# Kernel tuning notes

Hardware: AMD Instinct MI355X
Metric: run time of the kernel (lower is better)

The kernel has to match this reference:

```python
import jax, jax.numpy as jnp
from jax import lax
import numpy as np

MAX_K = 9  # alpha<1 -> kernel_size = 2*floor(floor(8*alpha)/2)+1 <= 9
SIGMA2 = 256.0  # sigma=16


def conv3x3(x, w, b):
    # reflection pad 1 + VALID 3x3 conv (torch cross-correlation == lax default)
    xp = jnp.pad(x, ((0, 0), (0, 0), (1, 1), (1, 1)), mode='reflect')
    y = lax.conv_general_dilated(xp, w, (1, 1), 'VALID')
    return y + b[None, :, None, None]


def up2(x):
    return jnp.repeat(jnp.repeat(x, 2, axis=2), 2, axis=3)


def get_hh(x):
    # x - nearest_upsample(avg_pool2(x)); H,W even
    B, C, H, W = x.shape
    p = x.reshape(B, C, H // 2, 2, W // 2, 2).mean(axis=(3, 5))
    return x - up2(p)


def feature_wct_simple(c, s, eps=1e-5):
    # AdaIN-style mean/std matching (torch.std_mean -> unbiased std, ddof=1)
    b, ch, h, w = c.shape
    cf = c.reshape(b, ch, -1)
    sf = s.reshape(b, ch, -1)
    cm = cf.mean(-1, keepdims=True)
    cs = jnp.std(cf, axis=-1, keepdims=True, ddof=1)
    sm = sf.mean(-1, keepdims=True)
    ss = jnp.std(sf, axis=-1, keepdims=True, ddof=1)
    return (((cf - cm) / (cs + eps)) * ss + sm).reshape(b, ch, h, w)


def gaussian_blur(x, alpha):
    # Per-sample dynamic kernel size k(alpha) embedded (zero-masked) in a fixed
    # MAX_K x MAX_K kernel with replicate pad MAX_K//2 -- exactly equivalent to
    # the original per-sample Conv2d with pad=(k-1)//2, but fully batched.
    B, C, H, W = x.shape
    cpos = MAX_K // 2
    k = jnp.floor(jnp.floor(alpha * 8.0) / 2.0) * 2.0 + 1.0  # [B]
    r = (k - 1.0) / 2.0  # per-sample radius
    coords = jnp.arange(MAX_K, dtype=jnp.float32) - cpos  # -4..4
    d2 = coords[:, None] ** 2 + coords[None, :] ** 2  # [9,9]
    g = jnp.exp(-d2 / (2.0 * SIGMA2))
    inr = jnp.abs(coords)[None, :] <= r[:, None]  # [B,9]
    mask = (inr[:, :, None] & inr[:, None, :]).astype(x.dtype)  # [B,9,9]
    ker = g[None] * mask
    ker = ker / jnp.sum(ker, axis=(1, 2), keepdims=True)  # [B,9,9]
    xp = jnp.pad(x, ((0, 0), (0, 0), (cpos, cpos), (cpos, cpos)), mode='edge')

    def one(xb, kb):  # depthwise conv, same 9x9 kernel for all channels
        w = jnp.broadcast_to(kb, (C, 1, MAX_K, MAX_K))
        return lax.conv_general_dilated(xb[None], w, (1, 1), 'VALID',
                                        feature_group_count=C)[0]

    return jax.vmap(one)(xp, ker)


def setup_inputs() -> dict:
    key = jax.random.key(0)
    ks = jax.random.split(key, 32)
    f = lambda i, s: jax.random.normal(ks[i], s, dtype=jnp.float32)
    inp = {
        'x': f(0, (4, 512, 32, 32)),
        'c34': f(1, (4, 256, 64, 64)),
        'c22': f(2, (4, 128, 128, 128)),
        'c12': f(3, (4, 64, 256, 256)),
        's34': f(4, (4, 256, 64, 64)),
        's31': f(5, (4, 256, 64, 64)),
        's22': f(6, (4, 128, 128, 128)),
        's21': f(7, (4, 128, 128, 128)),
        's12': f(8, (4, 64, 256, 256)),
        's11': f(9, (4, 64, 256, 256)),
        'alphas': jax.random.uniform(ks[10], (4, 3), dtype=jnp.float32),
        'w41': f(11, (256, 512, 3, 3)) * 0.05, 'b41': f(12, (256,)) * 0.05,
        'w34': f(13, (256, 256, 3, 3)) * 0.05, 'b34': f(14, (256,)) * 0.05,
        'w33': f(15, (256, 256, 3, 3)) * 0.05, 'b33': f(16, (256,)) * 0.05,
        'w32': f(17, (256, 256, 3, 3)) * 0.05, 'b32': f(18, (256,)) * 0.05,
        'w31': f(19, (128, 256, 3, 3)) * 0.05, 'b31': f(20, (128,)) * 0.05,
        'w22': f(21, (128, 128, 3, 3)) * 0.05, 'b22': f(22, (128,)) * 0.05,
        'w21': f(23, (64, 128, 3, 3)) * 0.05, 'b21': f(24, (64,)) * 0.05,
        'w12': f(25, (64, 64, 3, 3)) * 0.05, 'b12': f(26, (64,)) * 0.05,
        'w11': f(27, (3, 64, 3, 3)) * 0.05, 'b11': f(28, (3,)) * 0.05,
    }
    return inp


def reference(x, c34, c22, c12, s34, s31, s22, s21, s12, s11, alphas,
              w41, b41, w34, b34, w33, b33, w32, b32, w31, b31,
              w22, b22, w21, b21, w12, b12, w11, b11):
    relu = jax.nn.relu
    # level 4 -> 3
    out = relu(conv3x3(x, w41, b41))
    out = up2(out)  # to conv3_4 size
    out = out + gaussian_blur(get_hh(feature_wct_simple(c34, s34)), alphas[:, 2])
    out = relu(conv3x3(out, w34, b34))
    out = relu(conv3x3(out, w33, b33))
    out = relu(conv3x3(out, w32, b32))
    out = feature_wct_simple(out, s31)
    out = relu(conv3x3(out, w31, b31))
    # level 3 -> 2
    out = up2(out)  # to conv2_2 size
    out = out + gaussian_blur(get_hh(feature_wct_simple(c22, s22)), alphas[:, 1])
    out = relu(conv3x3(out, w22, b22))
    out = feature_wct_simple(out, s21)
    out = relu(conv3x3(out, w21, b21))
    # level 2 -> 1
    out = up2(out)  # to conv1_2 size
    out = out + gaussian_blur(get_hh(feature_wct_simple(c12, s12)), alphas[:, 0])
    out = relu(conv3x3(out, w12, b12))
    out = feature_wct_simple(out, s11)
    out = conv3x3(out, w11, b11)
    return out
```

## Files before the change

### kernel.cpp

```cpp
#include <hip/hip_runtime.h>
#include <math.h>

#define TPB 256

typedef __attribute__((ext_vector_type(8))) short s8v;
typedef __attribute__((ext_vector_type(4))) float f4v;

__device__ __forceinline__ unsigned bf16r(float f) {
  unsigned u = __float_as_uint(f);
  return (u + 0x7fffu + ((u >> 16) & 1u)) >> 16;
}

__global__ __launch_bounds__(128) void gauss1d_kernel(const float* __restrict__ alphas,
                                                      float* __restrict__ k1d) {
  int t = threadIdx.x;
  if (t >= 108) return;
  int lvl = t / 36;
  int rem = t - lvl * 36;
  int b = rem / 9;
  int j = rem - b * 9;
  float alpha = alphas[b * 3 + lvl];
  float k = floorf(floorf(alpha * 8.f) * 0.5f) * 2.f + 1.f;
  float r = (k - 1.f) * 0.5f;
  float sum = 0.f, val = 0.f;
  for (int u = 0; u < 9; ++u) {
    float d = (float)(u - 4);
    float g = expf(-(d * d) / 512.f);
    if (fabsf(d) > r) g = 0.f;
    if (u == j) val = g;
    sum += g;
  }
  k1d[(lvl * 4 + b) * 9 + j] = val / sum;
}

__global__ __launch_bounds__(TPB) void stats_kernel(const float* __restrict__ x,
                                                    float* __restrict__ mean,
                                                    float* __restrict__ stdv, int HW) {
  long long base = (long long)blockIdx.x * HW;
  float s = 0.f, q = 0.f;
  for (int i = threadIdx.x; i < HW; i += TPB) {
    float v = x[base + i];
    s += v;
    q = fmaf(v, v, q);
  }
#pragma unroll
  for (int off = 32; off > 0; off >>= 1) {
    s += __shfl_down(s, off, 64);
    q += __shfl_down(q, off, 64);
  }
  __shared__ float sm[8];
  int w = threadIdx.x >> 6, lane = threadIdx.x & 63;
  if (lane == 0) { sm[w * 2] = s; sm[w * 2 + 1] = q; }
  __syncthreads();
  if (threadIdx.x == 0) {
    float S = sm[0] + sm[2] + sm[4] + sm[6];
    float Q = sm[1] + sm[3] + sm[5] + sm[7];
    float m = S / (float)HW;
    float var = (Q - S * m) / (float)(HW - 1);
    mean[blockIdx.x] = m;
    stdv[blockIdx.x] = sqrtf(fmaxf(var, 0.f));
  }
}

__global__ __launch_bounds__(TPB) void pool2_kernel(const float* __restrict__ src,
                                                    float* __restrict__ dst,
                                                    int lwh, int lhh, long long n) {
  long long i = (long long)blockIdx.x * TPB + threadIdx.x;
  if (i >= n) return;
  int Wh = 1 << lwh, Hh = 1 << lhh;
  int px = (int)(i & (Wh - 1));
  int py = (int)((i >> lwh) & (Hh - 1));
  long long bc = i >> (lwh + lhh);
  const float* sp = src + (bc << (lwh + lhh + 2)) + (long long)(py * 2) * (Wh * 2) + px * 2;
  dst[i] = 0.25f * (sp[0] + sp[1] + sp[Wh * 2] + sp[Wh * 2 + 1]);
}

__global__ __launch_bounds__(TPB) void up2_kernel(const float* __restrict__ src,
                                                  float* __restrict__ dst,
                                                  int lw, int lh, long long n) {
  long long i = (long long)blockIdx.x * TPB + threadIdx.x;
  if (i >= n) return;
  int Wo = 1 << lw, Ho = 1 << lh;
  int x = (int)(i & (Wo - 1));
  int y = (int)((i >> lw) & (Ho - 1));
  long long bc = i >> (lw + lh);
  dst[i] = src[(bc << (lw + lh - 2)) + (long long)(y >> 1) * (Wo >> 1) + (x >> 1)];
}

__global__ __launch_bounds__(TPB) void blurx_kernel(const float* __restrict__ src,
                                                    const float* __restrict__ pmap,
                                                    const float* __restrict__ k1d,
                                                    float* __restrict__ dst,
                                                    int C, int lw, int lh) {
  int b = blockIdx.z;
  float kb[9];
#pragma unroll
  for (int t = 0; t < 9; ++t) kb[t] = k1d[b * 9 + t];
  int W = 1 << lw;
  long long i = (long long)blockIdx.x * TPB + threadIdx.x;
  long long nper = (long long)C << (lw + lh);
  if (i >= nper) return;
  int x = (int)(i & (W - 1));
  long long rest = i >> lw;
  int y = (int)(rest & ((1 << lh) - 1));
  int c = (int)(rest >> lh);
  long long bc = (long long)b * C + c;
  const float* sp = src + (bc << (lw + lh)) + ((long long)y << lw);
  const float* pp = pmap + (bc << (lw + lh - 2)) + ((long long)(y >> 1) << (lw - 1));
  float s = 0.f;
#pragma unroll
  for (int t = 0; t < 9; ++t) {
    int px = x + t - 4;
    px = px < 0 ? 0 : (px > W - 1 ? W - 1 : px);
    s = fmaf(kb[t], sp[px] - pp[px >> 1], s);
  }
  dst[(bc << (lw + lh)) + ((long long)y << lw) + x] = s;
}

__global__ __launch_bounds__(TPB) void blury_add_kernel(const float* __restrict__ tmp,
                                                        float* __restrict__ out,
                                                        const float* __restrict__ k1d,
                                                        const float* __restrict__ stdc,
                                                        const float* __restrict__ stds,
                                                        int C, int lw, int lh) {
  int b = blockIdx.z;
  float kb[9];
#pragma unroll
  for (int t = 0; t < 9; ++t) kb[t] = k1d[b * 9 + t];
  int W = 1 << lw, H = 1 << lh;
  long long i = (long long)blockIdx.x * TPB + threadIdx.x;
  long long nper = (long long)C << (lw + lh);
  if (i >= nper) return;
  int x = (int)(i & (W - 1));
  long long rest = i >> lw;
  int y = (int)(rest & (H - 1));
  int c = (int)(rest >> lh);
  int bc = b * C + c;
  float a = stds[bc] / (stdc[bc] + 1e-5f);
  const float* tp = tmp + ((long long)bc << (lw + lh)) + x;
  float s = 0.f;
#pragma unroll
  for (int t = 0; t < 9; ++t) {
    int py = y + t - 4;
    py = py < 0 ? 0 : (py > H - 1 ? H - 1 : py);
    s = fmaf(kb[t], tp[(long long)py << lw], s);
  }
  out[((long long)bc << (lw + lh)) + ((long long)y << lw) + x] += a * s;
}

__global__ __launch_bounds__(TPB) void affine_kernel(float* __restrict__ x,
                                                     const float* __restrict__ mc,
                                                     const float* __restrict__ sc,
                                                     const float* __restrict__ ms,
                                                     const float* __restrict__ ss, int HW) {
  int bc = blockIdx.y;
  float a = ss[bc] / (sc[bc] + 1e-5f);
  float d = ms[bc] - mc[bc] * a;
  long long base = (long long)bc * HW;
  for (int i = blockIdx.x * TPB + threadIdx.x; i < HW; i += gridDim.x * TPB)
    x[base + i] = fmaf(x[base + i], a, d);
}

__global__ __launch_bounds__(TPB) void bias_relu_kernel(float* __restrict__ x,
                                                        const float* __restrict__ bias,
                                                        int HW, int C, long long n) {
  long long i = (long long)blockIdx.x * TPB + threadIdx.x;
  if (i >= n) return;
  int c = (int)((i / HW) % C);
  x[i] = fmaxf(x[i] + bias[c], 0.f);
}

__global__ __launch_bounds__(TPB) void wsplit_kernel(const float* __restrict__ w,
                                                     short* __restrict__ wt,
                                                     int Cin, int Cout) {
  int nk = Cin >> 5, nc = Cout >> 4;
  int nf = 9 * nc * nk;
  int total = nf << 6;
  int planeStride = nf << 9;
  for (int i = blockIdx.x * TPB + threadIdx.x; i < total; i += gridDim.x * TPB) {
    int l = i & 63;
    int f = i >> 6;
    int cik = f % nk;
    int rem = f / nk;
    int cof = rem % nc;
    int t = rem / nc;
    int co = (cof << 4) + (l & 15);
    int ci = (cik << 5) + ((l >> 4) << 3);
    s8v hv, lv;
#pragma unroll
    for (int j = 0; j < 8; ++j) {
      float v = w[((long long)co * Cin + ci + j) * 9 + t];
      unsigned h = bf16r(v);
      float r = v - __uint_as_float(h << 16);
      hv[j] = (short)h;
      lv[j] = (short)bf16r(r);
    }
    long long o = ((long long)f << 9) + (l << 3);
    *(s8v*)(wt + o) = hv;
    *(s8v*)(wt + planeStride + o) = lv;
  }
}

template <bool RELU, bool ATOMIC>
__global__ __launch_bounds__(TPB, 3) void conv_mfma_kernel(
    const float* __restrict__ in, const short* __restrict__ wt,
    const float* __restrict__ bias, float* __restrict__ out,
    int Cin, int Cout, int H, int W, int ciPer, int ksplit) {
  __shared__ __align__(16) short sIn[2][12960];

  const int tid = threadIdx.x;
  const int l = tid & 63;
  const int wv = tid >> 6;
  const int xln = l & 15;
  const int kg = l >> 4;
  const int tilesX = W >> 4;
  const int tx0 = (blockIdx.x % tilesX) << 4;
  const int ty0 = (blockIdx.x / tilesX) << 4;
  const int co0 = blockIdx.y << 5;
  const int b = blockIdx.z / ksplit;
  const int kz = blockIdx.z % ksplit;
  const int ci0 = kz * ciPer;
  const long long HW = (long long)H * W;
  const long long inB = (long long)b * Cin * HW;

  const int nk = Cin >> 5;
  const int nc = Cout >> 4;
  const int planeStride = (9 * nc * nk) << 9;

  f4v acc[2][4];
#pragma unroll
  for (int m = 0; m < 2; ++m)
#pragma unroll
    for (int n = 0; n < 4; ++n) acc[m][n] = (f4v){0.f, 0.f, 0.f, 0.f};

  const int bOff = ((wv * 4) * 18 + xln) * 40 + kg * 8;

  for (int cc = 0; cc < ciPer; cc += 32) {
    const int cib = ci0 + cc;
    __syncthreads();
    for (int i = tid; i < 5184; i += TPB) {
      int ix = i % 18;
      int rem = i / 18;
      int cp = rem & 15;
      int iy = rem >> 4;
      int gy = ty0 - 1 + iy;
      gy = gy < 0 ? -gy : (gy >= H ? 2 * H - 2 - gy : gy);
      int gx = tx0 - 1 + ix;
      gx = gx < 0 ? -gx : (gx >= W ? 2 * W - 2 - gx : gx);
      long long gp = inB + (long long)(cib + cp * 2) * HW + (long long)gy * W + gx;
      float f0 = in[gp], f1 = in[gp + HW];
      unsigned h0 = bf16r(f0), h1 = bf16r(f1);
      unsigned lo0 = bf16r(f0 - __uint_as_float(h0 << 16));
      unsigned lo1 = bf16r(f1 - __uint_as_float(h1 << 16));
      int idx = (iy * 18 + ix) * 40 + cp * 2;
      *(unsigned*)&sIn[0][idx] = h0 | (h1 << 16);
      *(unsigned*)&sIn[1][idx] = lo0 | (lo1 << 16);
    }
    __syncthreads();

    const int cik = cib >> 5;
#pragma unroll
    for (int t = 0; t < 9; ++t) {
      const int r = t / 3, c = t % 3;
      s8v ah[2], al[2];
#pragma unroll
      for (int m = 0; m < 2; ++m) {
        int f = (t * nc + ((co0 >> 4) + m)) * nk + cik;
        const short* wp = wt + ((long long)f << 9) + (l << 3);
        ah[m] = *(const s8v*)wp;
        al[m] = *(const s8v*)(wp + planeStride);
      }
#pragma unroll
      for (int n = 0; n < 4; ++n) {
        int o = bOff + ((n + r) * 18 + c) * 40;
        s8v bh = *(const s8v*)&sIn[0][o];
        s8v bl = *(const s8v*)&sIn[1][o];
#pragma unroll
        for (int m = 0; m < 2; ++m) {
          acc[m][n] = __builtin_amdgcn_mfma_f32_16x16x32_bf16(ah[m], bh, acc[m][n], 0, 0, 0);
          acc[m][n] = __builtin_amdgcn_mfma_f32_16x16x32_bf16(ah[m], bl, acc[m][n], 0, 0, 0);
          acc[m][n] = __builtin_amdgcn_mfma_f32_16x16x32_bf16(al[m], bh, acc[m][n], 0, 0, 0);
        }
      }
    }
  }

#pragma unroll
  for (int m = 0; m < 2; ++m) {
    const int cb = co0 + m * 16 + kg * 4;
#pragma unroll
    for (int j = 0; j < 4; ++j) {
      const int co = cb + j;
      const float bv = ATOMIC ? 0.f : bias[co];
#pragma unroll
      for (int n = 0; n < 4; ++n) {
        long long oadr = ((long long)b * Cout + co) * HW +
                         (long long)(ty0 + wv * 4 + n) * W + tx0 + xln;
        float v = acc[m][n][j];
        if (ATOMIC) {
          atomicAdd(&out[oadr], v);
        } else {
          v += bv;
          if (RELU) v = fmaxf(v, 0.f);
          out[oadr] = v;
        }
      }
    }
  }
}

__global__ __launch_bounds__(TPB) void conv3x3_c3_kernel(
    const float* __restrict__ in, const float* __restrict__ wgt,
    const float* __restrict__ bias, float* __restrict__ out,
    int Cin, int H, int W) {
  __shared__ __align__(16) float tIn[8][18][20];
  const int tid = threadIdx.x;
  const int tilesX = W >> 4;
  const int tx0 = (blockIdx.x % tilesX) << 4;
  const int ty0 = (blockIdx.x / tilesX) << 4;
  const int b = blockIdx.z;
  const int tx = tid & 15, ty = tid >> 4;

  float acc[3] = {0.f, 0.f, 0.f};
  const long long inB = (long long)b * Cin * H * W;

  for (int cc = 0; cc < Cin; cc += 8) {
    __syncthreads();
    for (int i = tid; i < 8 * 324; i += TPB) {
      int ci = i / 324;
      int rem = i - ci * 324;
      int iy = rem / 18;
      int ix = rem - iy * 18;
      int gy = ty0 - 1 + iy;
      gy = gy < 0 ? -gy : (gy >= H ? 2 * H - 2 - gy : gy);
      int gx = tx0 - 1 + ix;
      gx = gx < 0 ? -gx : (gx >= W ? 2 * W - 2 - gx : gx);
      tIn[ci][iy][ix] = in[inB + (long long)(cc + ci) * H * W + (long long)gy * W + gx];
    }
    __syncthreads();
#pragma unroll 2
    for (int ci = 0; ci < 8; ++ci) {
#pragma unroll
      for (int r = 0; r < 3; ++r)
#pragma unroll
        for (int c = 0; c < 3; ++c) {
          float v = tIn[ci][ty + r][tx + c];
          int t = r * 3 + c;
          acc[0] = fmaf(wgt[((long long)(0 * Cin) + cc + ci) * 9 + t], v, acc[0]);
          acc[1] = fmaf(wgt[((long long)(1 * Cin) + cc + ci) * 9 + t], v, acc[1]);
          acc[2] = fmaf(wgt[((long long)(2 * Cin) + cc + ci) * 9 + t], v, acc[2]);
        }
    }
  }
  const long long HWl = (long long)H * W;
#pragma unroll
  for (int co = 0; co < 3; ++co)
    out[((long long)b * 3 + co) * HWl + (long long)(ty0 + ty) * W + tx0 + tx] =
        acc[co] + bias[co];
}

static inline void launch_conv_mfma(const float* in, const float* w, const float* bias,
                                    float* out, short* wsc, int Cin, int Cout,
                                    int H, int W, int ksplit, hipStream_t s) {
  int total = 9 * (Cout >> 4) * (Cin >> 5) * 64;
  int wgrid = (total + TPB - 1) / TPB;
  wsplit_kernel<<<wgrid, TPB, 0, s>>>(w, wsc, Cin, Cout);
  dim3 grid((W >> 4) * (H >> 4), Cout >> 5, 4 * ksplit);
  if (ksplit > 1)
    conv_mfma_kernel<false, true><<<grid, TPB, 0, s>>>(in, wsc, bias, out, Cin, Cout,
                                                       H, W, Cin / ksplit, ksplit);
  else
    conv_mfma_kernel<true, false><<<grid, TPB, 0, s>>>(in, wsc, bias, out, Cin, Cout,
                                                       H, W, Cin, 1);
}

extern "C" void kernel_launch(void* const* d_in, const int* in_sizes, int n_in,
                              void* d_out, int out_size, void* d_ws, size_t ws_size,
                              hipStream_t stream) {
  const float* x   = (const float*)d_in[0];
  const float* c34 = (const float*)d_in[1];
  const float* c22 = (const float*)d_in[2];
  const float* c12 = (const float*)d_in[3];
  const float* s34 = (const float*)d_in[4];
  const float* s31 = (const float*)d_in[5];
  const float* s22 = (const float*)d_in[6];
  const float* s21 = (const float*)d_in[7];
  const float* s12 = (const float*)d_in[8];
  const float* s11 = (const float*)d_in[9];
  const float* alphas = (const float*)d_in[10];
  const float* w41 = (const float*)d_in[11]; const float* b41 = (const float*)d_in[12];
  const float* w34 = (const float*)d_in[13]; const float* b34 = (const float*)d_in[14];
  const float* w33 = (const float*)d_in[15]; const float* b33 = (const float*)d_in[16];
  const float* w32 = (const float*)d_in[17]; const float* b32 = (const float*)d_in[18];
  const float* w31 = (const float*)d_in[19]; const float* b31 = (const float*)d_in[20];
  const float* w22 = (const float*)d_in[21]; const float* b22 = (const float*)d_in[22];
  const float* w21 = (const float*)d_in[23]; const float* b21 = (const float*)d_in[24];
  const float* w12 = (const float*)d_in[25]; const float* b12 = (const float*)d_in[26];
  const float* w11 = (const float*)d_in[27]; const float* b11 = (const float*)d_in[28];

  float* A  = (float*)d_ws;
  float* Bb = A + 16777216;
  float* P  = Bb + 16777216;
  float* mc = P + 4194304;
  float* sc = mc + 2048;
  float* ms = sc + 2048;
  float* ss = ms + 2048;
  float* k1 = ss + 2048;
  short* wsc = (short*)P;

  gauss1d_kernel<<<1, 128, 0, stream>>>(alphas, k1);

  hipMemsetAsync(A, 0, 4LL * 256 * 32 * 32 * 4, stream);
  launch_conv_mfma(x, w41, b41, A, wsc, 512, 256, 32, 32, 4, stream);
  {
    long long n = 4LL * 256 * 1024;
    bias_relu_kernel<<<(int)(n / TPB), TPB, 0, stream>>>(A, b41, 1024, 256, n);
  }
  {
    long long n = 4LL * 256 * 64 * 64;
    up2_kernel<<<(int)(n / TPB), TPB, 0, stream>>>(A, Bb, 6, 6, n);
  }
  stats_kernel<<<4 * 256, TPB, 0, stream>>>(c34, mc, sc, 64 * 64);
  stats_kernel<<<4 * 256, TPB, 0, stream>>>(s34, ms, ss, 64 * 64);
  {
    long long n = 4LL * 256 * 32 * 32;
    pool2_kernel<<<(int)(n / TPB), TPB, 0, stream>>>(c34, P, 5, 5, n);
  }
  {
    dim3 g((unsigned)((256LL * 64 * 64) / TPB), 1, 4);
    blurx_kernel<<<g, TPB, 0, stream>>>(c34, P, k1 + 72, A, 256, 6, 6);
    blury_add_kernel<<<g, TPB, 0, stream>>>(A, Bb, k1 + 72, sc, ss, 256, 6, 6);
  }
  launch_conv_mfma(Bb, w34, b34, A, wsc, 256, 256, 64, 64, 1, stream);
  launch_conv_mfma(A, w33, b33, Bb, wsc, 256, 256, 64, 64, 1, stream);
  launch_conv_mfma(Bb, w32, b32, A, wsc, 256, 256, 64, 64, 1, stream);
  stats_kernel<<<4 * 256, TPB, 0, stream>>>(A, mc, sc, 64 * 64);
  stats_kernel<<<4 * 256, TPB, 0, stream>>>(s31, ms, ss, 64 * 64);
  {
    dim3 g(16, 4 * 256);
    affine_kernel<<<g, TPB, 0, stream>>>(A, mc, sc, ms, ss, 64 * 64);
  }
  hipMemsetAsync(Bb, 0, 4LL * 128 * 64 * 64 * 4, stream);
  launch_conv_mfma(A, w31, b31, Bb, wsc, 256, 128, 64, 64, 2, stream);
  {
    long long n = 4LL * 128 * 4096;
    bias_relu_kernel<<<(int)(n / TPB), TPB, 0, stream>>>(Bb, b31, 4096, 128, n);
  }

  {
    long long n = 4LL * 128 * 128 * 128;
    up2_kernel<<<(int)(n / TPB), TPB, 0, stream>>>(Bb, A, 7, 7, n);
  }
  stats_kernel<<<4 * 128, TPB, 0, stream>>>(c22, mc, sc, 128 * 128);
  stats_kernel<<<4 * 128, TPB, 0, stream>>>(s22, ms, ss, 128 * 128);
  {
    long long n = 4LL * 128 * 64 * 64;
    pool2_kernel<<<(int)(n / TPB), TPB, 0, stream>>>(c22, P, 6, 6, n);
  }
  {
    dim3 g((unsigned)((128LL * 128 * 128) / TPB), 1, 4);
    blurx_kernel<<<g, TPB, 0, stream>>>(c22, P, k1 + 36, Bb, 128, 7, 7);
    blury_add_kernel<<<g, TPB, 0, stream>>>(Bb, A, k1 + 36, sc, ss, 128, 7, 7);
  }
  launch_conv_mfma(A, w22, b22, Bb, wsc, 128, 128, 128, 128, 1, stream);
  stats_kernel<<<4 * 128, TPB, 0, stream>>>(Bb, mc, sc, 128 * 128);
  stats_kernel<<<4 * 128, TPB, 0, stream>>>(s21, ms, ss, 128 * 128);
  {
    dim3 g(64, 4 * 128);
    affine_kernel<<<g, TPB, 0, stream>>>(Bb, mc, sc, ms, ss, 128 * 128);
  }
  launch_conv_mfma(Bb, w21, b21, A, wsc, 128, 64, 128, 128, 1, stream);

  {
    long long n = 4LL * 64 * 256 * 256;
    up2_kernel<<<(int)(n / TPB), TPB, 0, stream>>>(A, Bb, 8, 8, n);
  }
  stats_kernel<<<4 * 64, TPB, 0, stream>>>(c12, mc, sc, 256 * 256);
  stats_kernel<<<4 * 64, TPB, 0, stream>>>(s12, ms, ss, 256 * 256);
  {
    long long n = 4LL * 64 * 128 * 128;
    pool2_kernel<<<(int)(n / TPB), TPB, 0, stream>>>(c12, P, 7, 7, n);
  }
  {
    dim3 g((unsigned)((64LL * 256 * 256) / TPB), 1, 4);
    blurx_kernel<<<g, TPB, 0, stream>>>(c12, P, k1 + 0, A, 64, 8, 8);
    blury_add_kernel<<<g, TPB, 0, stream>>>(A, Bb, k1 + 0, sc, ss, 64, 8, 8);
  }
  launch_conv_mfma(Bb, w12, b12, A, wsc, 64, 64, 256, 256, 1, stream);
  stats_kernel<<<4 * 64, TPB, 0, stream>>>(A, mc, sc, 256 * 256);
  stats_kernel<<<4 * 64, TPB, 0, stream>>>(s11, ms, ss, 256 * 256);
  {
    dim3 g(256, 4 * 64);
    affine_kernel<<<g, TPB, 0, stream>>>(A, mc, sc, ms, ss, 256 * 256);
  }
  conv3x3_c3_kernel<<<dim3(256, 1, 4), TPB, 0, stream>>>(A, w11, b11, (float*)d_out,
                                                         64, 256, 256);
}
```

Measured before the change: 1.955 ms.

## Retile MFMA conv to 16x4 spatial by 64 channels with vectorized halo loads

The block tile moves from 16x16 pixels by 32 output channels to 16x4 pixels by 64 output channels. Each wave now owns 16 output channels across 4 rows and reuses B fragments across the three filter rows held in registers. Shared memory drops to about a third, so launch bounds are raised to 4 blocks per SM. Interior input loads use float4 with a separate halo-column path. The cost is more redundant halo reads per pixel and less weight reuse across rows, traded for better occupancy and finer grid granularity.

```diff
diff --git a/kernel.cpp b/kernel.cpp
--- a/kernel.cpp
+++ b/kernel.cpp
@@ -202,11 +202,11 @@
 }
 
 template <bool RELU, bool ATOMIC>
-__global__ __launch_bounds__(TPB, 3) void conv_mfma_kernel(
+__global__ __launch_bounds__(TPB, 4) void conv_mfma_kernel(
     const float* __restrict__ in, const short* __restrict__ wt,
     const float* __restrict__ bias, float* __restrict__ out,
     int Cin, int Cout, int H, int W, int ciPer, int ksplit) {
-  __shared__ __align__(16) short sIn[2][12960];
+  __shared__ __align__(16) short sIn[2][4320];
 
   const int tid = threadIdx.x;
   const int l = tid & 63;
@@ -215,8 +215,8 @@
   const int kg = l >> 4;
   const int tilesX = W >> 4;
   const int tx0 = (blockIdx.x % tilesX) << 4;
-  const int ty0 = (blockIdx.x / tilesX) << 4;
-  const int co0 = blockIdx.y << 5;
+  const int ty0 = (blockIdx.x / tilesX) << 2;
+  const int co0 = blockIdx.y << 6;
   const int b = blockIdx.z / ksplit;
   const int kz = blockIdx.z % ksplit;
   const int ci0 = kz * ciPer;
@@ -226,33 +226,53 @@
   const int nk = Cin >> 5;
   const int nc = Cout >> 4;
   const int planeStride = (9 * nc * nk) << 9;
-
-  f4v acc[2][4];
-#pragma unroll
-  for (int m = 0; m < 2; ++m)
-#pragma unroll
-    for (int n = 0; n < 4; ++n) acc[m][n] = (f4v){0.f, 0.f, 0.f, 0.f};
-
-  const int bOff = ((wv * 4) * 18 + xln) * 40 + kg * 8;
+  const int cof = (co0 >> 4) + wv;
+
+  f4v acc[4];
+#pragma unroll
+  for (int n = 0; n < 4; ++n) acc[n] = (f4v){0.f, 0.f, 0.f, 0.f};
 
   for (int cc = 0; cc < ciPer; cc += 32) {
     const int cib = ci0 + cc;
     __syncthreads();
-    for (int i = tid; i < 5184; i += TPB) {
-      int ix = i % 18;
-      int rem = i / 18;
-      int cp = rem & 15;
-      int iy = rem >> 4;
+    for (int i = tid; i < 384; i += TPB) {
+      int q = i & 3;
+      int cp = (i >> 2) & 15;
+      int iy = i >> 6;
       int gy = ty0 - 1 + iy;
       gy = gy < 0 ? -gy : (gy >= H ? 2 * H - 2 - gy : gy);
-      int gx = tx0 - 1 + ix;
+      int gx = tx0 + (q << 2);
+      long long gp = inB + (long long)(cib + cp * 2) * HW + (long long)gy * W + gx;
+      float4 f0 = *(const float4*)(in + gp);
+      float4 f1 = *(const float4*)(in + gp + HW);
+      float a0[4] = {f0.x, f0.y, f0.z, f0.w};
+      float a1[4] = {f1.x, f1.y, f1.z, f1.w};
+      int idx = (iy * 18 + 1 + (q << 2)) * 40 + cp * 2;
+#pragma unroll
+      for (int j = 0; j < 4; ++j) {
+        unsigned h0 = bf16r(a0[j]), h1 = bf16r(a1[j]);
+        float r0 = a0[j] - __uint_as_float(h0 << 16);
+        float r1 = a1[j] - __uint_as_float(h1 << 16);
+        unsigned lo0 = bf16r(r0), lo1 = bf16r(r1);
+        *(unsigned*)&sIn[0][idx + j * 40] = h0 | (h1 << 16);
+        *(unsigned*)&sIn[1][idx + j * 40] = lo0 | (lo1 << 16);
+      }
+    }
+    if (tid < 192) {
+      int col = tid & 1;
+      int cp = (tid >> 1) & 15;
+      int iy = tid >> 5;
+      int gy = ty0 - 1 + iy;
+      gy = gy < 0 ? -gy : (gy >= H ? 2 * H - 2 - gy : gy);
+      int gx = col ? tx0 + 16 : tx0 - 1;
       gx = gx < 0 ? -gx : (gx >= W ? 2 * W - 2 - gx : gx);
       long long gp = inB + (long long)(cib + cp * 2) * HW + (long long)gy * W + gx;
       float f0 = in[gp], f1 = in[gp + HW];
       unsigned h0 = bf16r(f0), h1 = bf16r(f1);
-      unsigned lo0 = bf16r(f0 - __uint_as_float(h0 << 16));
-      unsigned lo1 = bf16r(f1 - __uint_as_float(h1 << 16));
-      int idx = (iy * 18 + ix) * 40 + cp * 2;
+      float r0 = f0 - __uint_as_float(h0 << 16);
+      float r1 = f1 - __uint_as_float(h1 << 16);
+      unsigned lo0 = bf16r(r0), lo1 = bf16r(r1);
+      int idx = (iy * 18 + (col ? 17 : 0)) * 40 + cp * 2;
       *(unsigned*)&sIn[0][idx] = h0 | (h1 << 16);
       *(unsigned*)&sIn[1][idx] = lo0 | (lo1 << 16);
     }
@@ -260,50 +280,46 @@
 
     const int cik = cib >> 5;
 #pragma unroll
-    for (int t = 0; t < 9; ++t) {
-      const int r = t / 3, c = t % 3;
-      s8v ah[2], al[2];
-#pragma unroll
-      for (int m = 0; m < 2; ++m) {
-        int f = (t * nc + ((co0 >> 4) + m)) * nk + cik;
-        const short* wp = wt + ((long long)f << 9) + (l << 3);
-        ah[m] = *(const s8v*)wp;
-        al[m] = *(const s8v*)(wp + planeStride);
+    for (int c = 0; c < 3; ++c) {
+      s8v bh[6], bl[6];
+#pragma unroll
+      for (int ro = 0; ro < 6; ++ro) {
+        int o = (ro * 18 + xln + c) * 40 + kg * 8;
+        bh[ro] = *(const s8v*)&sIn[0][o];
+        bl[ro] = *(const s8v*)&sIn[1][o];
       }
 #pragma unroll
-      for (int n = 0; n < 4; ++n) {
-        int o = bOff + ((n + r) * 18 + c) * 40;
-        s8v bh = *(const s8v*)&sIn[0][o];
-        s8v bl = *(const s8v*)&sIn[1][o];
-#pragma unroll
-        for (int m = 0; m < 2; ++m) {
-          acc[m][n] = __builtin_amdgcn_mfma_f32_16x16x32_bf16(ah[m], bh, acc[m][n], 0, 0, 0);
-          acc[m][n] = __builtin_amdgcn_mfma_f32_16x16x32_bf16(ah[m], bl, acc[m][n], 0, 0, 0);
-          acc[m][n] = __builtin_amdgcn_mfma_f32_16x16x32_bf16(al[m], bh, acc[m][n], 0, 0, 0);
+      for (int r = 0; r < 3; ++r) {
+        const int t = r * 3 + c;
+        const long long f = (long long)(t * nc + cof) * nk + cik;
+        const short* wp = wt + (f << 9) + (l << 3);
+        s8v ah = *(const s8v*)wp;
+        s8v al = *(const s8v*)(wp + planeStride);
+#pragma unroll
+        for (int n = 0; n < 4; ++n) {
+          acc[n] = __builtin_amdgcn_mfma_f32_16x16x32_bf16(ah, bh[n + r], acc[n], 0, 0, 0);
+          acc[n] = __builtin_amdgcn_mfma_f32_16x16x32_bf16(ah, bl[n + r], acc[n], 0, 0, 0);
+          acc[n] = __builtin_amdgcn_mfma_f32_16x16x32_bf16(al, bh[n + r], acc[n], 0, 0, 0);
         }
       }
     }
   }
 
-#pragma unroll
-  for (int m = 0; m < 2; ++m) {
-    const int cb = co0 + m * 16 + kg * 4;
-#pragma unroll
-    for (int j = 0; j < 4; ++j) {
-      const int co = cb + j;
-      const float bv = ATOMIC ? 0.f : bias[co];
-#pragma unroll
-      for (int n = 0; n < 4; ++n) {
-        long long oadr = ((long long)b * Cout + co) * HW +
-                         (long long)(ty0 + wv * 4 + n) * W + tx0 + xln;
-        float v = acc[m][n][j];
-        if (ATOMIC) {
-          atomicAdd(&out[oadr], v);
-        } else {
-          v += bv;
-          if (RELU) v = fmaxf(v, 0.f);
-          out[oadr] = v;
-        }
+  const int cb = co0 + wv * 16 + kg * 4;
+#pragma unroll
+  for (int j = 0; j < 4; ++j) {
+    const int co = cb + j;
+    const float bv = ATOMIC ? 0.f : bias[co];
+    float* op = out + ((long long)b * Cout + co) * HW + (long long)ty0 * W + tx0 + xln;
+#pragma unroll
+    for (int n = 0; n < 4; ++n) {
+      float v = acc[n][j];
+      if (ATOMIC) {
+        atomicAdd(op + (long long)n * W, v);
+      } else {
+        v += bv;
+        if (RELU) v = fmaxf(v, 0.f);
+        op[(long long)n * W] = v;
       }
     }
   }
@@ -365,7 +381,7 @@
   int total = 9 * (Cout >> 4) * (Cin >> 5) * 64;
   int wgrid = (total + TPB - 1) / TPB;
   wsplit_kernel<<<wgrid, TPB, 0, s>>>(w, wsc, Cin, Cout);
-  dim3 grid((W >> 4) * (H >> 4), Cout >> 5, 4 * ksplit);
+  dim3 grid((W >> 4) * (H >> 2), Cout >> 6, 4 * ksplit);
   if (ksplit > 1)
     conv_mfma_kernel<false, true><<<grid, TPB, 0, s>>>(in, wsc, bias, out, Cin, Cout,
                                                        H, W, Cin / ksplit, ksplit);
```

New measurement: 1.697 ms. 1.15x faster.
